# Kernel tuning notes

Measured on AMD Instinct MI355X. Metric: run time of the kernel, lower is better.

The kernel has to match this reference:

```python
import jax, jax.numpy as jnp
import numpy as np

# Static tree structure: B jets, each a perfect binary tree of depth DEPTH.
B = 64
DEPTH = 12                       # levels 0..DEPTH; level j has B*2**j nodes
N_FEAT = 7
N_HID = 128
LEVEL_SIZES = [B * (1 << j) for j in range(DEPTH + 1)]
OFFSETS = np.concatenate([[0], np.cumsum(LEVEL_SIZES)]).astype(np.int64).tolist()
TOTAL = OFFSETS[-1]              # 524224 nodes
INNER_SIZES = LEVEL_SIZES[:-1]   # all nodes inner except leaf level
INNER_OFF = np.concatenate([[0], np.cumsum(INNER_SIZES)]).astype(np.int64).tolist()


def setup_inputs() -> dict:
    key = jax.random.key(0)
    k_c, k_wu, k_wh = jax.random.split(key, 3)
    contents = jax.random.normal(k_c, (TOTAL, N_FEAT), dtype=jnp.float32)
    # children: per level j < DEPTH, a random pairing (permutation) of level j+1 nodes
    rng = np.random.default_rng(0)
    ch = []
    for j in range(DEPTH):
        perm = rng.permutation(LEVEL_SIZES[j + 1]).astype(np.int32)
        ch.append(perm.reshape(LEVEL_SIZES[j], 2))
    children = jnp.asarray(np.concatenate(ch, axis=0))  # [262080, 2]
    # Learned params (torch nn.Linear: y = x @ W.T + b)
    w_u = jax.random.normal(k_wu, (N_HID, N_FEAT), dtype=jnp.float32) / np.float32(np.sqrt(N_FEAT))
    b_u = jnp.zeros((N_HID,), jnp.float32)
    w_h = jax.random.normal(k_wh, (N_HID, 3 * N_HID), dtype=jnp.float32) / np.float32(np.sqrt(3 * N_HID))
    b_h = jnp.zeros((N_HID,), jnp.float32)
    return {"contents": contents, "children": children,
            "w_u": w_u, "b_u": b_u, "w_h": w_h, "b_h": b_h}


def reference(contents, children, w_u, b_u, w_h, b_h):
    # Bottom-up pass over tree levels (leaves -> root), mirroring the torch loop
    # over levels[::-1]. Perfect binary tree: every non-leaf node is inner.
    emb = None
    for j in range(DEPTH, -1, -1):
        c_j = contents[OFFSETS[j]:OFFSETS[j + 1]]              # [B*2^j, F]
        u = jnp.tanh(c_j @ w_u.T + b_u)                        # [B*2^j, H]
        if j < DEPTH:
            ch_j = children[INNER_OFF[j]:INNER_OFF[j + 1]]     # [B*2^j, 2]
            h_L = emb[ch_j[:, 0]]                              # gather from prev level
            h_R = emb[ch_j[:, 1]]
            emb = jnp.tanh(jnp.concatenate([h_L, h_R, u], axis=1) @ w_h.T + b_h)
        else:
            emb = u  # leaf level: no inner nodes
    return emb.reshape(B, -1)  # root embedding per jet: [B, N_HID]
```

## Files before the change

kernel.cpp:

```cpp
#include <hip/hip_runtime.h>
#include <hip/hip_bf16.h>


#define NF 7
#define NH 128
#define XSTR 136
#define XSTR3 392

typedef __bf16 bf16;
typedef __bf16 bf16x8 __attribute__((ext_vector_type(8)));
typedef float floatx16 __attribute__((ext_vector_type(16)));
typedef float floatx2 __attribute__((ext_vector_type(2)));

__device__ __forceinline__ float ftanh(float x){
    float e = __builtin_amdgcn_exp2f(x * 2.8853900817779268f);
    return fmaf(-2.0f, __builtin_amdgcn_rcpf(e + 1.0f), 1.0f);
}

__device__ __forceinline__ floatx2 pkfma(float c, floatx2 w, floatx2 a){
    floatx2 cc = {c, c};
    return __builtin_elementwise_fma(cc, w, a);
}

__global__ __launch_bounds__(256) void k_prep0(
    const int2* __restrict__ children,
    const float* __restrict__ w_u, const float* __restrict__ b_u,
    const float* __restrict__ w_h,
    int* __restrict__ ids_A, int* __restrict__ ids_B,
    bf16* __restrict__ wb, bf16* __restrict__ w_ub)
{
    const int t = threadIdx.x;
    const int b = blockIdx.x;
    if (b < 4){
        int root = b * 256 + t;
        int* base = ids_A + root * 128;
        const int2* ch4 = children + 960;
        const int2* ch5 = children + 1984;
        const int2* ch6 = children + 4032;
        const int2* ch7 = children + 8128;
        const int2* ch8 = children + 16320;
        const int2* ch9 = children + 32704;
        int l5[2], l6[4], l7[8], l8[16], l9[32];
        { int2 c = ch4[root]; l5[0] = c.x; l5[1] = c.y; }
        #pragma unroll
        for (int k = 0; k < 2; ++k){ int2 c = ch5[l5[k]]; l6[2*k] = c.x; l6[2*k+1] = c.y; }
        #pragma unroll
        for (int k = 0; k < 4; ++k){ int2 c = ch6[l6[k]]; l7[2*k] = c.x; l7[2*k+1] = c.y; }
        #pragma unroll
        for (int k = 0; k < 8; ++k){ int2 c = ch7[l7[k]]; l8[2*k] = c.x; l8[2*k+1] = c.y; }
        #pragma unroll
        for (int k = 0; k < 16; ++k){ int2 c = ch8[l8[k]]; l9[2*k] = c.x; l9[2*k+1] = c.y; }
        base[0] = root;
        base[1] = l5[0]; base[2] = l5[1];
        #pragma unroll
        for (int k = 0; k < 4; ++k)  base[3 + k]  = l6[k];
        #pragma unroll
        for (int k = 0; k < 8; ++k)  base[7 + k]  = l7[k];
        #pragma unroll
        for (int k = 0; k < 16; ++k) base[15 + k] = l8[k];
        #pragma unroll
        for (int k = 0; k < 32; ++k) base[31 + k] = l9[k];
        #pragma unroll
        for (int k = 0; k < 32; ++k){
            int2 c = ch9[l9[k]];
            base[63 + 2*k] = c.x; base[64 + 2*k] = c.y;
        }
    } else if (b == 4){
        if (t < 64){
            int root = t;
            int* base = ids_B + root * 32;
            const int2* ch0 = children;
            const int2* ch1 = children + 64;
            const int2* ch2 = children + 192;
            const int2* ch3 = children + 448;
            int l1[2], l2[4], l3[8];
            { int2 c = ch0[root]; l1[0] = c.x; l1[1] = c.y; }
            #pragma unroll
            for (int k = 0; k < 2; ++k){ int2 c = ch1[l1[k]]; l2[2*k] = c.x; l2[2*k+1] = c.y; }
            #pragma unroll
            for (int k = 0; k < 4; ++k){ int2 c = ch2[l2[k]]; l3[2*k] = c.x; l3[2*k+1] = c.y; }
            base[0] = root;
            base[1] = l1[0]; base[2] = l1[1];
            #pragma unroll
            for (int k = 0; k < 4; ++k) base[3 + k] = l2[k];
            #pragma unroll
            for (int k = 0; k < 8; ++k) base[7 + k] = l3[k];
            #pragma unroll
            for (int k = 0; k < 8; ++k){
                int2 c = ch3[l3[k]];
                base[15 + 2*k] = c.x; base[16 + 2*k] = c.y;
            }
        } else if (t < 192){
            int col = t - 64;
            union { uint4 u4[2]; bf16 h[16]; } row;
            #pragma unroll
            for (int f = 0; f < NF; ++f) row.h[f] = (bf16)w_u[col * NF + f];
            row.h[7] = (bf16)b_u[col];
            #pragma unroll
            for (int k = 8; k < 16; ++k) row.h[k] = (bf16)0.0f;
            *(uint4*)&w_ub[col * 16]     = row.u4[0];
            *(uint4*)&w_ub[col * 16 + 8] = row.u4[1];
        }
    } else {
        int idx = (b - 5) * 256 + t;
        wb[idx] = (bf16)w_h[idx];
    }
}

__global__ __launch_bounds__(256, 2) void k_lvl11(
    const float* __restrict__ contents, const int2* __restrict__ children,
    const float* __restrict__ w_u, const float* __restrict__ b_u,
    const bf16* __restrict__ w_ub, const bf16* __restrict__ wb,
    const float* __restrict__ b_h, bf16* __restrict__ emb11,
    unsigned int* __restrict__ usm_u32)
{
    __shared__ bf16 xs[64 * XSTR3];
    __shared__ int chS[128];
    const int t = threadIdx.x;
    const int b = blockIdx.x;

    if (b >= 2048){
        float* csL = (float*)xs;
        const size_t srow = (size_t)(b - 2048) * 128;
        if (t < 224){
            float4 v = ((const float4*)(contents + srow * NF))[t];
            int e = t * 4;
            float vv[4] = {v.x, v.y, v.z, v.w};
            #pragma unroll
            for (int r = 0; r < 4; ++r){ int ee = e + r; csL[(ee/7)*8 + (ee%7)] = vv[r]; }
        }
        const int cp = t & 63;
        const int quarter = t >> 6;
        floatx2 wu2[NF];
        {
            const float* w0 = w_u + (size_t)(2 * cp) * NF;
            #pragma unroll
            for (int f = 0; f < NF; ++f){ floatx2 w = {w0[f], w0[NF + f]}; wu2[f] = w; }
        }
        floatx2 bu2 = {b_u[2 * cp], b_u[2 * cp + 1]};
        __syncthreads();
        #pragma unroll 4
        for (int i = 0; i < 32; ++i){
            int node = quarter * 32 + i;
            float4 c0 = *(const float4*)&csL[node * 8];
            float4 c1 = *(const float4*)&csL[node * 8 + 4];
            floatx2 a = bu2;
            a = pkfma(c0.x, wu2[0], a);
            a = pkfma(c0.y, wu2[1], a);
            a = pkfma(c0.z, wu2[2], a);
            a = pkfma(c0.w, wu2[3], a);
            a = pkfma(c1.x, wu2[4], a);
            a = pkfma(c1.y, wu2[5], a);
            a = pkfma(c1.z, wu2[6], a);
            union { unsigned int u; bf16 h[2]; } pk;
            pk.h[0] = (bf16)ftanh(a[0]);
            pk.h[1] = (bf16)ftanh(a[1]);
            usm_u32[(srow + node) * 64 + cp] = pk.u;
        }
        return;
    }

    const int node0 = b * 64;
    const int2* ch11 = children + 131008;
    const float* cont11 = contents + (size_t)131008 * NF;
    const float* contL  = contents + (size_t)262080 * NF;

    if (t < 64){ int2 c = ch11[node0 + t]; chS[2*t] = c.x; chS[2*t + 1] = c.y; }

    const int lane = t & 63;
    const int ct = t >> 6;
    const int m = lane & 31;
    const int q = lane >> 5;
    const int colg = ct * 32 + m;
    const bf16x8 bu = *(const bf16x8*)(w_ub + (size_t)colg * 16 + q * 8);
    __syncthreads();

    float rows[6][NF];
    if (q == 0){
        #pragma unroll
        for (int tile = 0; tile < 6; ++tile){
            const float* src;
            if (tile < 4) src = contL + (size_t)chS[tile * 32 + m] * NF;
            else          src = cont11 + (size_t)(node0 + (tile - 4) * 32 + m) * NF;
            #pragma unroll
            for (int f = 0; f < NF; ++f) rows[tile][f] = src[f];
        }
    }

    #pragma unroll
    for (int tile = 0; tile < 6; ++tile){
        bf16x8 a = {bf16(0.f),bf16(0.f),bf16(0.f),bf16(0.f),
                    bf16(0.f),bf16(0.f),bf16(0.f),bf16(0.f)};
        if (q == 0){
            union { bf16x8 v; bf16 h[8]; } u8;
            #pragma unroll
            for (int f = 0; f < NF; ++f) u8.h[f] = (bf16)rows[tile][f];
            u8.h[7] = (bf16)1.0f;
            a = u8.v;
        }
        floatx16 acc = {0,0,0,0,0,0,0,0,0,0,0,0,0,0,0,0};
        acc = __builtin_amdgcn_mfma_f32_32x32x16_bf16(a, bu, acc, 0, 0, 0);
        #pragma unroll
        for (int r = 0; r < 16; ++r){
            int row = (r & 3) + 8 * (r >> 2) + 4 * q;
            bf16 hv = (bf16)ftanh(acc[r]);
            if (tile < 4){
                int c = tile * 32 + row;
                xs[(c >> 1) * XSTR3 + (c & 1) * 128 + colg] = hv;
            } else {
                int i = (tile - 4) * 32 + row;
                xs[i * XSTR3 + 256 + colg] = hv;
            }
        }
    }
    __syncthreads();

    floatx16 acc0 = {0,0,0,0,0,0,0,0,0,0,0,0,0,0,0,0};
    floatx16 acc1 = {0,0,0,0,0,0,0,0,0,0,0,0,0,0,0,0};
    const bf16* bq = wb + (size_t)colg * 384 + q * 8;
    const bf16* xa = &xs[m * XSTR3 + q * 8];
    #pragma unroll
    for (int grp = 0; grp < 3; ++grp){
        bf16x8 bfr[8];
        #pragma unroll
        for (int kk = 0; kk < 8; ++kk)
            bfr[kk] = *(const bf16x8*)(bq + grp * 128 + kk * 16);
        #pragma unroll
        for (int kk = 0; kk < 8; ++kk){
            bf16x8 a0 = *(const bf16x8*)(xa + grp * 128 + kk * 16);
            bf16x8 a1 = *(const bf16x8*)(xa + grp * 128 + kk * 16 + 32 * XSTR3);
            acc0 = __builtin_amdgcn_mfma_f32_32x32x16_bf16(a0, bfr[kk], acc0, 0, 0, 0);
            acc1 = __builtin_amdgcn_mfma_f32_32x32x16_bf16(a1, bfr[kk], acc1, 0, 0, 0);
        }
    }

    const float bv = b_h[colg];
    #pragma unroll
    for (int nt = 0; nt < 2; ++nt){
        const floatx16* accp = nt ? &acc1 : &acc0;
        #pragma unroll
        for (int r = 0; r < 16; ++r){
            int row  = (r & 3) + 8 * (r >> 2) + 4 * q;
            int node = node0 + nt * 32 + row;
            emb11[(size_t)node * NH + colg] = (bf16)ftanh((*accp)[r] + bv);
        }
    }
}

__global__ __launch_bounds__(256, 4) void k_inner(
    const int2* __restrict__ children, const float* __restrict__ contents,
    const float* __restrict__ w_u, const float* __restrict__ b_u,
    const bf16* __restrict__ wb, const float* __restrict__ b_h,
    const bf16* __restrict__ emb_next, bf16* __restrict__ out_b)
{
    __shared__ bf16 xs[64 * XSTR];
    __shared__ int2 ch_s[64];
    __shared__ float cs[64 * 8];
    const int t = threadIdx.x;
    const int block0 = blockIdx.x * 64;
    if (t < 64) ch_s[t] = children[block0 + t];
    if (t < 112){
        float4 v = ((const float4*)(contents + (size_t)block0 * NF))[t];
        int e = t * 4;
        float vv[4] = {v.x, v.y, v.z, v.w};
        #pragma unroll
        for (int r = 0; r < 4; ++r){ int ee = e + r; cs[(ee/7)*8 + (ee%7)] = vv[r]; }
    }
    const int cp = t & 63;
    const int quarter = t >> 6;
    floatx2 wu2[NF];
    {
        const float* w0 = w_u + (size_t)(2 * cp) * NF;
        #pragma unroll
        for (int f = 0; f < NF; ++f){ floatx2 w = {w0[f], w0[NF + f]}; wu2[f] = w; }
    }
    floatx2 bu2 = {b_u[2 * cp], b_u[2 * cp + 1]};
    const int lane = t & 63;
    const int ct = t >> 6;
    const int m = lane & 31;
    const int q = lane >> 5;
    floatx16 acc0 = {0,0,0,0,0,0,0,0,0,0,0,0,0,0,0,0};
    floatx16 acc1 = {0,0,0,0,0,0,0,0,0,0,0,0,0,0,0,0};
    const bf16* bq = wb + ((size_t)(ct * 32 + m) * 384 + q * 8);
    #pragma unroll 1
    for (int p = 0; p < 3; ++p){
        __syncthreads();
        if (p < 2){
            #pragma unroll
            for (int r = 0; r < 4; ++r){
                int task = r * 256 + t;
                int i = task >> 4, part = task & 15;
                int row = (p == 0) ? ch_s[i].x : ch_s[i].y;
                uint4 v = *(const uint4*)(emb_next + (size_t)row * NH + part * 8);
                *(uint4*)&xs[i * XSTR + part * 8] = v;
            }
        } else {
            #pragma unroll 4
            for (int i = 0; i < 16; ++i){
                int node = quarter * 16 + i;
                float4 c0 = *(const float4*)&cs[node * 8];
                float4 c1 = *(const float4*)&cs[node * 8 + 4];
                floatx2 a = bu2;
                a = pkfma(c0.x, wu2[0], a);
                a = pkfma(c0.y, wu2[1], a);
                a = pkfma(c0.z, wu2[2], a);
                a = pkfma(c0.w, wu2[3], a);
                a = pkfma(c1.x, wu2[4], a);
                a = pkfma(c1.y, wu2[5], a);
                a = pkfma(c1.z, wu2[6], a);
                union { unsigned int u; bf16 h[2]; } pk;
                pk.h[0] = (bf16)ftanh(a[0]);
                pk.h[1] = (bf16)ftanh(a[1]);
                ((unsigned int*)xs)[node * (XSTR / 2) + cp] = pk.u;
            }
        }
        bf16x8 bfr[8];
        #pragma unroll
        for (int kk = 0; kk < 8; ++kk)
            bfr[kk] = *(const bf16x8*)(bq + p * 128 + kk * 16);
        __syncthreads();
        const bf16* xa = &xs[m * XSTR + q * 8];
        #pragma unroll
        for (int kk = 0; kk < 8; ++kk){
            bf16x8 a0 = *(const bf16x8*)(xa + kk * 16);
            bf16x8 a1 = *(const bf16x8*)(xa + kk * 16 + 32 * XSTR);
            acc0 = __builtin_amdgcn_mfma_f32_32x32x16_bf16(a0, bfr[kk], acc0, 0, 0, 0);
            acc1 = __builtin_amdgcn_mfma_f32_32x32x16_bf16(a1, bfr[kk], acc1, 0, 0, 0);
        }
    }
    const int colg = ct * 32 + m;
    const float bv = b_h[colg];
    #pragma unroll
    for (int nt = 0; nt < 2; ++nt){
        const floatx16* accp = nt ? &acc1 : &acc0;
        #pragma unroll
        for (int r = 0; r < 16; ++r){
            int row  = (r & 3) + 8 * (r >> 2) + 4 * q;
            int node = block0 + nt * 32 + row;
            out_b[(size_t)node * NH + colg] = (bf16)ftanh((*accp)[r] + bv);
        }
    }
}

__global__ __launch_bounds__(256, 2) void k_tailA(
    const int* __restrict__ ids_A, const bf16* __restrict__ u_small,
    const bf16* __restrict__ wb, const float* __restrict__ b_h,
    const bf16* __restrict__ emb10, bf16* __restrict__ emb4)
{
    __shared__ bf16 xs[32 * XSTR3];
    __shared__ bf16 embL[32 * 136];
    __shared__ int ids[128];
    const int t = threadIdx.x, root = blockIdx.x;
    const int ct = t >> 6, lane = t & 63, m = lane & 31, q = lane >> 5;
    const float bv = b_h[ct * 32 + m];
    if (t < 32) ((uint4*)ids)[t] = ((const uint4*)(ids_A + root * 128))[t];
    __syncthreads();
    const bf16* bq = wb + ((size_t)(ct * 32 + m) * 384 + q * 8);

    bf16x8 bfr[3][8];
    #pragma unroll
    for (int grp = 0; grp < 3; ++grp)
        #pragma unroll
        for (int kk = 0; kk < 8; ++kk)
            bfr[grp][kk] = *(const bf16x8*)(bq + grp * 128 + kk * 16);

    #pragma unroll 1
    for (int l = 9; l >= 4; --l){
        const int n = 1 << (l - 4);
        #pragma unroll 1
        for (int r = 0; r < 4; ++r){
            int task = r * 256 + t;
            if (task < n * 32){
                int i = task >> 5, half = (task >> 4) & 1, part = task & 15;
                uint4 v;
                if (l == 9) v = *(const uint4*)(emb10 + (size_t)ids[63 + 2*i + half] * NH + part * 8);
                else        v = *(uint4*)&embL[(2*i + half) * 136 + part * 8];
                *(uint4*)&xs[i * XSTR3 + half * 128 + part * 8] = v;
            }
        }
        #pragma unroll 1
        for (int r = 0; r < 2; ++r){
            int task = r * 256 + t;
            if (task < n * 16){
                int i = task >> 4, part = task & 15;
                size_t row = (size_t)64 * ((1u << l) - 1) + ids[(n - 1) + i];
                *(uint4*)&xs[i * XSTR3 + 256 + part * 8] =
                    *(const uint4*)(u_small + row * NH + part * 8);
            }
        }
        __syncthreads();
        floatx16 accs[3];
        #pragma unroll
        for (int g = 0; g < 3; ++g) accs[g] = (floatx16){0,0,0,0,0,0,0,0,0,0,0,0,0,0,0,0};
        const bf16* xa = &xs[m * XSTR3 + q * 8];
        #pragma unroll
        for (int grp = 0; grp < 3; ++grp){
            #pragma unroll
            for (int kk = 0; kk < 8; ++kk){
                bf16x8 a0 = *(const bf16x8*)(xa + grp * 128 + kk * 16);
                accs[grp] = __builtin_amdgcn_mfma_f32_32x32x16_bf16(a0, bfr[grp][kk], accs[grp], 0, 0, 0);
            }
        }
        floatx16 acc = accs[0] + accs[1] + accs[2];
        __syncthreads();
        #pragma unroll
        for (int r = 0; r < 16; ++r){
            int row = (r & 3) + 8 * (r >> 2) + 4 * q;
            if (row < n){
                float v = ftanh(acc[r] + bv);
                if (l > 4) embL[row * 136 + ct * 32 + m] = (bf16)v;
                else       emb4[(size_t)root * NH + ct * 32 + m] = (bf16)v;
            }
        }
        __syncthreads();
    }
}

__global__ __launch_bounds__(256, 2) void k_tailB(
    const int* __restrict__ ids_B, const bf16* __restrict__ u_small,
    const bf16* __restrict__ wb, const float* __restrict__ b_h,
    const bf16* __restrict__ emb4, float* __restrict__ out_f)
{
    __shared__ bf16 xs[8 * XSTR3];
    __shared__ bf16 embL[8 * 136];
    __shared__ int ids[32];
    const int t = threadIdx.x, root = blockIdx.x;
    const int ct = t >> 6, lane = t & 63, m = lane & 31, q = lane >> 5;
    const float bv = b_h[ct * 32 + m];
    if (t < 8) ((uint4*)ids)[t] = ((const uint4*)(ids_B + root * 32))[t];
    __syncthreads();
    const bf16* bq = wb + ((size_t)(ct * 32 + m) * 384 + q * 8);

    bf16x8 bfr[3][8];
    #pragma unroll
    for (int grp = 0; grp < 3; ++grp)
        #pragma unroll
        for (int kk = 0; kk < 8; ++kk)
            bfr[grp][kk] = *(const bf16x8*)(bq + grp * 128 + kk * 16);

    #pragma unroll 1
    for (int l = 3; l >= 0; --l){
        const int n = 1 << l;
        {
            int task = t;
            if (task < n * 32){
                int i = task >> 5, half = (task >> 4) & 1, part = task & 15;
                uint4 v;
                if (l == 3) v = *(const uint4*)(emb4 + (size_t)ids[15 + 2*i + half] * NH + part * 8);
                else        v = *(uint4*)&embL[(2*i + half) * 136 + part * 8];
                *(uint4*)&xs[i * XSTR3 + half * 128 + part * 8] = v;
            }
            if (task < n * 16){
                int i = task >> 4, part = task & 15;
                size_t row = (size_t)64 * ((1u << l) - 1) + ids[(n - 1) + i];
                *(uint4*)&xs[i * XSTR3 + 256 + part * 8] =
                    *(const uint4*)(u_small + row * NH + part * 8);
            }
        }
        __syncthreads();
        floatx16 accs[3];
        #pragma unroll
        for (int g = 0; g < 3; ++g) accs[g] = (floatx16){0,0,0,0,0,0,0,0,0,0,0,0,0,0,0,0};
        const bf16* xa = &xs[m * XSTR3 + q * 8];
        #pragma unroll
        for (int grp = 0; grp < 3; ++grp){
            #pragma unroll
            for (int kk = 0; kk < 8; ++kk){
                bf16x8 a0 = *(const bf16x8*)(xa + grp * 128 + kk * 16);
                accs[grp] = __builtin_amdgcn_mfma_f32_32x32x16_bf16(a0, bfr[grp][kk], accs[grp], 0, 0, 0);
            }
        }
        floatx16 acc = accs[0] + accs[1] + accs[2];
        __syncthreads();
        #pragma unroll
        for (int r = 0; r < 16; ++r){
            int row = (r & 3) + 8 * (r >> 2) + 4 * q;
            if (row < n){
                float v = ftanh(acc[r] + bv);
                if (l > 0) embL[row * 136 + ct * 32 + m] = (bf16)v;
                else       out_f[(size_t)root * NH + ct * 32 + m] = v;
            }
        }
        __syncthreads();
    }
}

extern "C" void kernel_launch(void* const* d_in, const int* in_sizes, int n_in,
                              void* d_out, int out_size, void* d_ws, size_t ws_size,
                              hipStream_t stream){
    const float* contents = (const float*)d_in[0];
    const int2*  children = (const int2*)d_in[1];
    const float* w_u      = (const float*)d_in[2];
    const float* b_u      = (const float*)d_in[3];
    const float* w_h      = (const float*)d_in[4];
    const float* b_h      = (const float*)d_in[5];
    float* outf = (float*)d_out;

    bf16* embA    = (bf16*)d_ws;
    bf16* embB    = embA + (size_t)65536 * NH;
    bf16* wb      = embB + (size_t)131072 * NH;
    bf16* u_small = wb + (size_t)NH * 384;
    int*  ids_A   = (int*)(u_small + (size_t)65536 * NH);
    int*  ids_B   = ids_A + 1024 * 128;
    bf16* w_ub    = (bf16*)(ids_B + 64 * 32);

    hipLaunchKernelGGL(k_prep0, dim3(197), dim3(256), 0, stream,
                       children, w_u, b_u, w_h, ids_A, ids_B, wb, w_ub);
    hipLaunchKernelGGL(k_lvl11, dim3(2560), dim3(256), 0, stream,
                       contents, children, w_u, b_u, w_ub, wb, b_h,
                       embB, (unsigned int*)u_small);
    hipLaunchKernelGGL(k_inner, dim3(1024), dim3(256), 0, stream,
                       children + 65472, contents + (size_t)65472 * NF,
                       w_u, b_u, wb, b_h, embB, embA);
    hipLaunchKernelGGL(k_tailA, dim3(1024), dim3(256), 0, stream,
                       ids_A, u_small, wb, b_h, embA, embB);
    hipLaunchKernelGGL(k_tailB, dim3(64), dim3(256), 0, stream,
                       ids_B, u_small, wb, b_h, embB, outf);
}
```

Baseline: 203.9 us.

## Shrink lvl11 shared buffer to one K-slice and stage slices through registers

The level-11 kernel previously held the full 64x384 concatenated [hL,hR,u] activation tile in LDS. It now keeps only one 128-wide slice in LDS, holds the other two in registers, and refills the buffer between the three K-groups with extra barriers. This cuts LDS per block by about two thirds, so launch bounds are raised from 2 to 4 blocks per CU for more occupancy. The cost is extra register pressure, more __syncthreads, and serialized write/compute phases.

```diff
diff --git a/kernel.cpp b/kernel.cpp
--- a/kernel.cpp
+++ b/kernel.cpp
@@ -107,14 +107,14 @@
     }
 }
 
-__global__ __launch_bounds__(256, 2) void k_lvl11(
+__global__ __launch_bounds__(256, 4) void k_lvl11(
     const float* __restrict__ contents, const int2* __restrict__ children,
     const float* __restrict__ w_u, const float* __restrict__ b_u,
     const bf16* __restrict__ w_ub, const bf16* __restrict__ wb,
     const float* __restrict__ b_h, bf16* __restrict__ emb11,
     unsigned int* __restrict__ usm_u32)
 {
-    __shared__ bf16 xs[64 * XSTR3];
+    __shared__ bf16 xs[64 * XSTR];
     __shared__ int chS[128];
     const int t = threadIdx.x;
     const int b = blockIdx.x;
@@ -187,6 +187,8 @@
         }
     }
 
+    bf16 oddv[4][8];
+    bf16 ownv[2][16];
     #pragma unroll
     for (int tile = 0; tile < 6; ++tile){
         bf16x8 a = {bf16(0.f),bf16(0.f),bf16(0.f),bf16(0.f),
@@ -206,31 +208,52 @@
             bf16 hv = (bf16)ftanh(acc[r]);
             if (tile < 4){
                 int c = tile * 32 + row;
-                xs[(c >> 1) * XSTR3 + (c & 1) * 128 + colg] = hv;
+                if ((r & 1) == 0) xs[(c >> 1) * XSTR + colg] = hv;
+                else              oddv[tile][r >> 1] = hv;
             } else {
-                int i = (tile - 4) * 32 + row;
-                xs[i * XSTR3 + 256 + colg] = hv;
-            }
-        }
-    }
-    __syncthreads();
+                ownv[tile - 4][r] = hv;
+            }
+        }
+    }
 
     floatx16 acc0 = {0,0,0,0,0,0,0,0,0,0,0,0,0,0,0,0};
     floatx16 acc1 = {0,0,0,0,0,0,0,0,0,0,0,0,0,0,0,0};
     const bf16* bq = wb + (size_t)colg * 384 + q * 8;
-    const bf16* xa = &xs[m * XSTR3 + q * 8];
+    const bf16* xa = &xs[m * XSTR + q * 8];
     #pragma unroll
-    for (int grp = 0; grp < 3; ++grp){
+    for (int p = 0; p < 3; ++p){
         bf16x8 bfr[8];
         #pragma unroll
         for (int kk = 0; kk < 8; ++kk)
-            bfr[kk] = *(const bf16x8*)(bq + grp * 128 + kk * 16);
+            bfr[kk] = *(const bf16x8*)(bq + p * 128 + kk * 16);
+        __syncthreads();
         #pragma unroll
         for (int kk = 0; kk < 8; ++kk){
-            bf16x8 a0 = *(const bf16x8*)(xa + grp * 128 + kk * 16);
-            bf16x8 a1 = *(const bf16x8*)(xa + grp * 128 + kk * 16 + 32 * XSTR3);
+            bf16x8 a0 = *(const bf16x8*)(xa + kk * 16);
+            bf16x8 a1 = *(const bf16x8*)(xa + kk * 16 + 32 * XSTR);
             acc0 = __builtin_amdgcn_mfma_f32_32x32x16_bf16(a0, bfr[kk], acc0, 0, 0, 0);
             acc1 = __builtin_amdgcn_mfma_f32_32x32x16_bf16(a1, bfr[kk], acc1, 0, 0, 0);
+        }
+        if (p < 2){
+            __syncthreads();
+            if (p == 0){
+                #pragma unroll
+                for (int tile = 0; tile < 4; ++tile)
+                    #pragma unroll
+                    for (int j = 0; j < 8; ++j){
+                        int r = 2 * j + 1;
+                        int row = (r & 3) + 8 * (r >> 2) + 4 * q;
+                        xs[(tile * 16 + (row >> 1)) * XSTR + colg] = oddv[tile][j];
+                    }
+            } else {
+                #pragma unroll
+                for (int tt = 0; tt < 2; ++tt)
+                    #pragma unroll
+                    for (int r = 0; r < 16; ++r){
+                        int row = (r & 3) + 8 * (r >> 2) + 4 * q;
+                        xs[(tt * 32 + row) * XSTR + colg] = ownv[tt][r];
+                    }
+            }
         }
     }
 
```

After: 201.6 us. About the same (-1.1%).

## Compute leaf-projection u on the fly in tail kernels instead of precomputing

Applied to the files above, without the earlier changes.

Removes the extra 512 blocks of k_lvl11 that precomputed tanh(W_u c) for the small levels (0-9) into a u_small buffer. The tail kernels instead gather each node's 7 contents features and compute the 128-wide u row directly into shared memory. This drops a 16 MB bf16 intermediate write and its read-back, at the cost of redundant small FMAs and tanh inside the latency-bound tail kernels. It also adds register pressure there from the W_u weights.

```diff
diff --git a/kernel.cpp b/kernel.cpp
--- a/kernel.cpp
+++ b/kernel.cpp
@@ -109,56 +109,13 @@
 
 __global__ __launch_bounds__(256, 2) void k_lvl11(
     const float* __restrict__ contents, const int2* __restrict__ children,
-    const float* __restrict__ w_u, const float* __restrict__ b_u,
     const bf16* __restrict__ w_ub, const bf16* __restrict__ wb,
-    const float* __restrict__ b_h, bf16* __restrict__ emb11,
-    unsigned int* __restrict__ usm_u32)
+    const float* __restrict__ b_h, bf16* __restrict__ emb11)
 {
     __shared__ bf16 xs[64 * XSTR3];
     __shared__ int chS[128];
     const int t = threadIdx.x;
     const int b = blockIdx.x;
-
-    if (b >= 2048){
-        float* csL = (float*)xs;
-        const size_t srow = (size_t)(b - 2048) * 128;
-        if (t < 224){
-            float4 v = ((const float4*)(contents + srow * NF))[t];
-            int e = t * 4;
-            float vv[4] = {v.x, v.y, v.z, v.w};
-            #pragma unroll
-            for (int r = 0; r < 4; ++r){ int ee = e + r; csL[(ee/7)*8 + (ee%7)] = vv[r]; }
-        }
-        const int cp = t & 63;
-        const int quarter = t >> 6;
-        floatx2 wu2[NF];
-        {
-            const float* w0 = w_u + (size_t)(2 * cp) * NF;
-            #pragma unroll
-            for (int f = 0; f < NF; ++f){ floatx2 w = {w0[f], w0[NF + f]}; wu2[f] = w; }
-        }
-        floatx2 bu2 = {b_u[2 * cp], b_u[2 * cp + 1]};
-        __syncthreads();
-        #pragma unroll 4
-        for (int i = 0; i < 32; ++i){
-            int node = quarter * 32 + i;
-            float4 c0 = *(const float4*)&csL[node * 8];
-            float4 c1 = *(const float4*)&csL[node * 8 + 4];
-            floatx2 a = bu2;
-            a = pkfma(c0.x, wu2[0], a);
-            a = pkfma(c0.y, wu2[1], a);
-            a = pkfma(c0.z, wu2[2], a);
-            a = pkfma(c0.w, wu2[3], a);
-            a = pkfma(c1.x, wu2[4], a);
-            a = pkfma(c1.y, wu2[5], a);
-            a = pkfma(c1.z, wu2[6], a);
-            union { unsigned int u; bf16 h[2]; } pk;
-            pk.h[0] = (bf16)ftanh(a[0]);
-            pk.h[1] = (bf16)ftanh(a[1]);
-            usm_u32[(srow + node) * 64 + cp] = pk.u;
-        }
-        return;
-    }
 
     const int node0 = b * 64;
     const int2* ch11 = children + 131008;
@@ -343,7 +300,8 @@
 }
 
 __global__ __launch_bounds__(256, 2) void k_tailA(
-    const int* __restrict__ ids_A, const bf16* __restrict__ u_small,
+    const int* __restrict__ ids_A, const float* __restrict__ contents,
+    const float* __restrict__ w_u, const float* __restrict__ b_u,
     const bf16* __restrict__ wb, const float* __restrict__ b_h,
     const bf16* __restrict__ emb10, bf16* __restrict__ emb4)
 {
@@ -352,10 +310,18 @@
     __shared__ int ids[128];
     const int t = threadIdx.x, root = blockIdx.x;
     const int ct = t >> 6, lane = t & 63, m = lane & 31, q = lane >> 5;
+    const int cp = t & 63;
     const float bv = b_h[ct * 32 + m];
     if (t < 32) ((uint4*)ids)[t] = ((const uint4*)(ids_A + root * 128))[t];
-    __syncthreads();
     const bf16* bq = wb + ((size_t)(ct * 32 + m) * 384 + q * 8);
+
+    floatx2 wu2[NF];
+    {
+        const float* w0 = w_u + (size_t)(2 * cp) * NF;
+        #pragma unroll
+        for (int f = 0; f < NF; ++f){ floatx2 w = {w0[f], w0[NF + f]}; wu2[f] = w; }
+    }
+    const floatx2 bu2 = {b_u[2 * cp], b_u[2 * cp + 1]};
 
     bf16x8 bfr[3][8];
     #pragma unroll
@@ -363,6 +329,7 @@
         #pragma unroll
         for (int kk = 0; kk < 8; ++kk)
             bfr[grp][kk] = *(const bf16x8*)(bq + grp * 128 + kk * 16);
+    __syncthreads();
 
     #pragma unroll 1
     for (int l = 9; l >= 4; --l){
@@ -379,13 +346,24 @@
             }
         }
         #pragma unroll 1
-        for (int r = 0; r < 2; ++r){
+        for (int r = 0; r < 8; ++r){
             int task = r * 256 + t;
-            if (task < n * 16){
-                int i = task >> 4, part = task & 15;
+            if (task < n * 64){
+                int i = task >> 6;
                 size_t row = (size_t)64 * ((1u << l) - 1) + ids[(n - 1) + i];
-                *(uint4*)&xs[i * XSTR3 + 256 + part * 8] =
-                    *(const uint4*)(u_small + row * NH + part * 8);
+                const float* src = contents + row * NF;
+                floatx2 a = bu2;
+                a = pkfma(src[0], wu2[0], a);
+                a = pkfma(src[1], wu2[1], a);
+                a = pkfma(src[2], wu2[2], a);
+                a = pkfma(src[3], wu2[3], a);
+                a = pkfma(src[4], wu2[4], a);
+                a = pkfma(src[5], wu2[5], a);
+                a = pkfma(src[6], wu2[6], a);
+                union { unsigned int u; bf16 h[2]; } pk;
+                pk.h[0] = (bf16)ftanh(a[0]);
+                pk.h[1] = (bf16)ftanh(a[1]);
+                *(unsigned int*)&xs[i * XSTR3 + 256 + 2 * cp] = pk.u;
             }
         }
         __syncthreads();
@@ -417,7 +395,8 @@
 }
 
 __global__ __launch_bounds__(256, 2) void k_tailB(
-    const int* __restrict__ ids_B, const bf16* __restrict__ u_small,
+    const int* __restrict__ ids_B, const float* __restrict__ contents,
+    const float* __restrict__ w_u, const float* __restrict__ b_u,
     const bf16* __restrict__ wb, const float* __restrict__ b_h,
     const bf16* __restrict__ emb4, float* __restrict__ out_f)
 {
@@ -426,10 +405,18 @@
     __shared__ int ids[32];
     const int t = threadIdx.x, root = blockIdx.x;
     const int ct = t >> 6, lane = t & 63, m = lane & 31, q = lane >> 5;
+    const int cp = t & 63;
     const float bv = b_h[ct * 32 + m];
     if (t < 8) ((uint4*)ids)[t] = ((const uint4*)(ids_B + root * 32))[t];
-    __syncthreads();
     const bf16* bq = wb + ((size_t)(ct * 32 + m) * 384 + q * 8);
+
+    floatx2 wu2[NF];
+    {
+        const float* w0 = w_u + (size_t)(2 * cp) * NF;
+        #pragma unroll
+        for (int f = 0; f < NF; ++f){ floatx2 w = {w0[f], w0[NF + f]}; wu2[f] = w; }
+    }
+    const floatx2 bu2 = {b_u[2 * cp], b_u[2 * cp + 1]};
 
     bf16x8 bfr[3][8];
     #pragma unroll
@@ -437,6 +424,7 @@
         #pragma unroll
         for (int kk = 0; kk < 8; ++kk)
             bfr[grp][kk] = *(const bf16x8*)(bq + grp * 128 + kk * 16);
+    __syncthreads();
 
     #pragma unroll 1
     for (int l = 3; l >= 0; --l){
@@ -450,11 +438,26 @@
                 else        v = *(uint4*)&embL[(2*i + half) * 136 + part * 8];
                 *(uint4*)&xs[i * XSTR3 + half * 128 + part * 8] = v;
             }
-            if (task < n * 16){
-                int i = task >> 4, part = task & 15;
+        }
+        #pragma unroll 1
+        for (int r = 0; r < 2; ++r){
+            int task = r * 256 + t;
+            if (task < n * 64){
+                int i = task >> 6;
                 size_t row = (size_t)64 * ((1u << l) - 1) + ids[(n - 1) + i];
-                *(uint4*)&xs[i * XSTR3 + 256 + part * 8] =
-                    *(const uint4*)(u_small + row * NH + part * 8);
+                const float* src = contents + row * NF;
+                floatx2 a = bu2;
+                a = pkfma(src[0], wu2[0], a);
+                a = pkfma(src[1], wu2[1], a);
+                a = pkfma(src[2], wu2[2], a);
+                a = pkfma(src[3], wu2[3], a);
+                a = pkfma(src[4], wu2[4], a);
+                a = pkfma(src[5], wu2[5], a);
+                a = pkfma(src[6], wu2[6], a);
+                union { unsigned int u; bf16 h[2]; } pk;
+                pk.h[0] = (bf16)ftanh(a[0]);
+                pk.h[1] = (bf16)ftanh(a[1]);
+                *(unsigned int*)&xs[i * XSTR3 + 256 + 2 * cp] = pk.u;
             }
         }
         __syncthreads();
@@ -499,21 +502,19 @@
     bf16* embA    = (bf16*)d_ws;
     bf16* embB    = embA + (size_t)65536 * NH;
     bf16* wb      = embB + (size_t)131072 * NH;
-    bf16* u_small = wb + (size_t)NH * 384;
-    int*  ids_A   = (int*)(u_small + (size_t)65536 * NH);
+    int*  ids_A   = (int*)(wb + (size_t)NH * 384);
     int*  ids_B   = ids_A + 1024 * 128;
     bf16* w_ub    = (bf16*)(ids_B + 64 * 32);
 
     hipLaunchKernelGGL(k_prep0, dim3(197), dim3(256), 0, stream,
                        children, w_u, b_u, w_h, ids_A, ids_B, wb, w_ub);
-    hipLaunchKernelGGL(k_lvl11, dim3(2560), dim3(256), 0, stream,
-                       contents, children, w_u, b_u, w_ub, wb, b_h,
-                       embB, (unsigned int*)u_small);
+    hipLaunchKernelGGL(k_lvl11, dim3(2048), dim3(256), 0, stream,
+                       contents, children, w_ub, wb, b_h, embB);
     hipLaunchKernelGGL(k_inner, dim3(1024), dim3(256), 0, stream,
                        children + 65472, contents + (size_t)65472 * NF,
                        w_u, b_u, wb, b_h, embB, embA);
     hipLaunchKernelGGL(k_tailA, dim3(1024), dim3(256), 0, stream,
-                       ids_A, u_small, wb, b_h, embA, embB);
+                       ids_A, contents, w_u, b_u, wb, b_h, embA, embB);
     hipLaunchKernelGGL(k_tailB, dim3(64), dim3(256), 0, stream,
-                       ids_B, u_small, wb, b_h, embB, outf);
-}
+                       ids_B, contents, w_u, b_u, wb, b_h, embB, outf);
+}
```

New measurement: 210.5 us. +3.2%, slower.
